# Kernel optimization log

Hardware: AMD Instinct MI355X
Metric: run time of the kernel (lower is better)

## Reference

```python
import jax, jax.numpy as jnp
import numpy as np

N_HIDDEN = 15


def lstm_cell(x, h, c, W_ih, W_hh, b_ih, b_hh):
    # x: [B, in], h/c: [B, H]. PyTorch LSTMCell gate order: i, f, g, o
    gates = x @ W_ih.T + h @ W_hh.T + b_ih + b_hh  # [B, 4H]
    i, f, g, o = jnp.split(gates, 4, axis=-1)
    i = jax.nn.sigmoid(i)
    f = jax.nn.sigmoid(f)
    g = jnp.tanh(g)
    o = jax.nn.sigmoid(o)
    c_new = f * c + i * g
    h_new = o * jnp.tanh(c_new)
    return h_new, c_new


def setup_inputs() -> dict:
    key = jax.random.key(0)
    ks = jax.random.split(key, 12)
    B, T, H = 4096, 1024, N_HIDDEN
    s = 1.0 / np.sqrt(H)  # torch default init bound
    u = lambda k, shape: jax.random.uniform(k, shape, jnp.float32, -s, s)
    return {
        "input": jax.random.normal(ks[0], (B, T), jnp.float32),
        "W_ih1": u(ks[1], (4 * H, 1)),
        "W_hh1": u(ks[2], (4 * H, H)),
        "b_ih1": u(ks[3], (4 * H,)),
        "b_hh1": u(ks[4], (4 * H,)),
        "W_ih2": u(ks[5], (4 * H, H)),
        "W_hh2": u(ks[6], (4 * H, H)),
        "b_ih2": u(ks[7], (4 * H,)),
        "b_hh2": u(ks[8], (4 * H,)),
        "W_lin": u(ks[9], (1, H)),
        "b_lin": u(ks[10], (1,)),
        "future": 64,
    }


def reference(input, W_ih1, W_hh1, b_ih1, b_hh1, W_ih2, W_hh2, b_ih2, b_hh2, W_lin, b_lin, future):
    B = input.shape[0]
    H = N_HIDDEN
    zeros = jnp.zeros((B, H), input.dtype)

    def step(carry, x_t):
        h1, c1, h2, c2 = carry
        h1, c1 = lstm_cell(x_t, h1, c1, W_ih1, W_hh1, b_ih1, b_hh1)
        h2, c2 = lstm_cell(h1, h2, c2, W_ih2, W_hh2, b_ih2, b_hh2)
        out = h2 @ W_lin.T + b_lin  # [B, 1]
        return (h1, c1, h2, c2), out

    xs = input.T[:, :, None]  # [T, B, 1]
    carry, outs = jax.lax.scan(step, (zeros, zeros, zeros, zeros), xs)

    last_out = outs[-1]  # [B, 1]

    def fut_step(carry, _):
        h1, c1, h2, c2, out = carry
        (h1, c1, h2, c2), out = step((h1, c1, h2, c2), out)
        return (h1, c1, h2, c2, out), out

    _, fut_outs = jax.lax.scan(fut_step, (*carry, last_out), None, length=future)

    all_outs = jnp.concatenate([outs, fut_outs], axis=0)  # [T+future, B, 1]
    return all_outs[:, :, 0].T  # [B, T+future]
```

## Files before the change

### kernel.cpp

```cpp
#include <hip/hip_runtime.h>

#define HID   15
#define TMAIN 1024
#define FUT   64
#define OUTW  (TMAIN + FUT)

typedef _Float16 v2h   __attribute__((ext_vector_type(2)));
typedef _Float16 v8h   __attribute__((ext_vector_type(8)));
typedef float    f32x4 __attribute__((ext_vector_type(4)));
typedef int      i32x4 __attribute__((ext_vector_type(4)));

__device__ __forceinline__ float rcp_(float x)  { return __builtin_amdgcn_rcpf(x); }
__device__ __forceinline__ float exp2_(float x) { return __builtin_amdgcn_exp2f(x); }

template<int I> struct ic { static constexpr int v = I; };
template<int J, int N, class F>
__device__ __forceinline__ void unroll_for(F&& f) {
    if constexpr (J < N) { f(ic<J>{}); unroll_for<J + 1, N>(f); }
}

template<int PAT>
__device__ __forceinline__ int swzi(int x) { return __builtin_amdgcn_ds_swizzle(x, PAT); }
template<int PAT>
__device__ __forceinline__ float swzf(float x) { return __int_as_float(swzi<PAT>(__float_as_int(x))); }

__device__ __forceinline__ int bpermi(int addr, int x) { return __builtin_amdgcn_ds_bpermute(addr, x); }
__device__ __forceinline__ float bpermf(int addr, float x) { return __int_as_float(bpermi(addr, __float_as_int(x))); }

template<int CTRL>
__device__ __forceinline__ int dppi(int x) {
    return __builtin_amdgcn_update_dpp(0, x, CTRL, 0xF, 0xF, true);
}

__device__ __forceinline__ v2h pkrtz(float lo, float hi) {
    return __builtin_bit_cast(v2h, __builtin_amdgcn_cvt_pkrtz(lo, hi));
}
__device__ __forceinline__ f32x4 mfma16(v8h a, v8h b, f32x4 c) {
    return __builtin_amdgcn_mfma_f32_16x16x32_f16(a, b, c, 0, 0, 0);
}
template<int I>
__device__ __forceinline__ float xel(const f32x4& a, const f32x4& b) {
    if constexpr (I < 4) return a[I]; else return b[I - 4];
}

__global__ __launch_bounds__(256)
__attribute__((amdgpu_waves_per_eu(1, 1)))
void lstm_seq_kernel(const float* __restrict__ input,
                     const float* __restrict__ W_ih1, const float* __restrict__ W_hh1,
                     const float* __restrict__ b_ih1, const float* __restrict__ b_hh1,
                     const float* __restrict__ W_ih2, const float* __restrict__ W_hh2,
                     const float* __restrict__ b_ih2, const float* __restrict__ b_hh2,
                     const float* __restrict__ W_lin, const float* __restrict__ b_lin,
                     float* __restrict__ out)
{
    const int tid  = threadIdx.x;
    const int wq   = tid >> 6;
    const int lane = tid & 63;
    const int u    = lane >> 4;
    const int c    = lane & 15;
    const int s    = c & 3;
    const int cg   = c >> 2;
    const int b0   = (blockIdx.x * 4 + wq) * 4;

    const float L2E = 1.442695040888963f;
    const float sA[4] = {-L2E, -L2E, -2.0f * L2E, -L2E};
    const float blin = b_lin[0];

    v8h   A1[4], A2[4];
    f32x4 C1[4], C2[4];
    #pragma unroll
    for (int m = 0; m < 4; ++m) {
        #pragma unroll
        for (int e = 0; e < 8; ++e) {
            const int k = (e < 4) ? (4 * u + e) : (16 + 4 * u + (e - 4));
            float v1 = 0.0f, v2 = 0.0f;
            if (c < HID) {
                const int wr = m * HID + c;
                if (k < HID)       { v1 = W_hh1[wr * HID + k]; v2 = W_ih2[wr * HID + k]; }
                else if (k == HID) { v1 = W_ih1[wr]; }
                else if (k >= 16 && k < 16 + HID) { v2 = W_hh2[wr * HID + (k - 16)]; }
            }
            float a2v = sA[m] * v2;
            if (c == 15 && m == 3 && k >= 16 && k < 16 + HID)
                a2v = W_lin[k - 16];
            A1[m][e] = (_Float16)(sA[m] * v1);
            A2[m][e] = (_Float16)a2v;
        }
        #pragma unroll
        for (int r = 0; r < 4; ++r) {
            const int U = 4 * u + r;
            float bv1 = 0.0f, bv2 = 0.0f;
            if (U < HID) {
                bv1 = sA[m] * (b_ih1[m * HID + U] + b_hh1[m * HID + U]);
                bv2 = sA[m] * (b_ih2[m * HID + U] + b_hh2[m * HID + U]);
            }
            if (u == 3 && m == 3 && r == 3) bv2 = blin;
            C1[m][r] = bv1; C2[m][r] = bv2;
        }
    }

    const int   Uown = 4 * u + cg;
    const float wl2  = (Uown < HID) ? W_lin[Uown] : 0.0f;

    const bool cgb0  = (cg & 1) != 0;
    const bool cgb1  = (cg & 2) != 0;
    const bool u3b   = (u == 3);
    const int  a32   = (lane ^ 32) << 2;

    int B0 = 0, B1 = 0;
    int B2s = 0, B3s = 0;
    int B2f = 0, B3f = 0;
    float c1v = 0.0f, c2v = 0.0f;
    float oA = 0.0f, oB = 0.0f;

    auto gsel = [&](const f32x4& q0, const f32x4& q1, const f32x4& q2, const f32x4& q3,
                    float& g0, float& g1, float& g2, float& g3) {
        auto pick = [&](const f32x4& q) -> float {
            const float t0 = cgb0 ? q[1] : q[0];
            const float t1 = cgb0 ? q[3] : q[2];
            return cgb1 ? t1 : t0;
        };
        g0 = pick(q0); g1 = pick(q1); g2 = pick(q2); g3 = pick(q3);
    };

    auto acts = [&](float g0, float g1, float g2, float g3, float& cv) -> float {
        const float Ei = exp2_(g0);
        const float Ef = exp2_(g1);
        const float Eg = exp2_(g2);
        const float Eo = exp2_(g3);
        const float Di = 1.0f + Ei;
        const float Df = 1.0f + Ef;
        const float Dg = 1.0f + Eg;
        const float P  = Di * Dg;
        const float t  = __builtin_fmaf(-Eg, Df, Df);
        const float numer = __builtin_fmaf(cv, P, t);
        cv = numer * rcp_(P * Df);
        const float Y  = exp2_(cv * -2.885390081777927f);
        return (1.0f - Y) * rcp_((1.0f + Y) * (1.0f + Eo));
    };

    auto slots = [&](float h, float& s0, float& s1, float& s2, float& s3) {
        const int hb = __float_as_int(h);
        const float r4  = __int_as_float(dppi<0x114>(hb) | dppi<0x10C>(hb));
        const float r8  = __int_as_float(dppi<0x118>(hb) | dppi<0x108>(hb));
        const float r12 = __int_as_float(dppi<0x11C>(hb) | dppi<0x104>(hb));
        const float A0 = cgb0 ? r4  : h;
        const float A1 = cgb0 ? r12 : r8;
        const float A2 = cgb0 ? h   : r12;
        const float A3 = cgb0 ? r8  : r4;
        s0 = cgb1 ? A1 : A0;
        s1 = cgb1 ? A3 : A2;
        s2 = cgb1 ? A0 : A1;
        s3 = cgb1 ? A2 : A3;
    };

    auto pack01 = [&](float h1n, float xv) {
        float s0, s1, s2, s3; slots(h1n, s0, s1, s2, s3);
        B0 = __builtin_bit_cast(int, pkrtz(s0, s1));
        B1 = __builtin_bit_cast(int, pkrtz(s2, u3b ? xv : s3));
    };
    auto pack23 = [&](float h2n) {
        const int hb = __float_as_int(h2n);
        const float hr = __int_as_float(dppi<0x104>(hb));
        const int p = __builtin_bit_cast(int, pkrtz(h2n, hr));
        B2f = swzi<0x0013>(p);
        B3f = swzi<0x0113>(p);
    };

    auto stash = [&](auto SigC, float ov) {
        constexpr int SIG = decltype(SigC)::v;
        const bool own = (cg == (SIG & 3));
        if constexpr (SIG < 4) oA = own ? ov : oA;
        else                   oB = own ? ov : oB;
    };

    const size_t xadr   = (size_t)(b0 + s) * TMAIN;
    const size_t outb_o = (size_t)(b0 + s) * OUTW;

    auto storeChunk = [&](int chIdx, int baseOff) {
        if (u3b) {
            out[outb_o + baseOff + (size_t)chIdx * 8 + cg]     = oA;
            out[outb_o + baseOff + (size_t)chIdx * 8 + 4 + cg] = oB;
        }
    };

    auto outdot = [&](float h) -> float {
        float pv = wl2 * h;
        pv += swzf<0x101F>(pv);
        pv += swzf<0x201F>(pv);
        pv += swzf<0x401F>(pv);
        pv += bpermf(a32, pv);
        return pv + blin;
    };

    auto iterP = [&](auto Sc, float xv2) {
        constexpr int S = decltype(Sc)::v;
        const v8h Bd = __builtin_bit_cast(v8h, (i32x4){B0, B1, B2s, B3s});
        f32x4 d0 = mfma16(A1[0], Bd, C1[0]);
        f32x4 d1 = mfma16(A1[1], Bd, C1[1]);
        f32x4 d2 = mfma16(A1[2], Bd, C1[2]);
        f32x4 d3 = mfma16(A1[3], Bd, C1[3]);
        const v8h Be = __builtin_bit_cast(v8h, (i32x4){B0, B1, B2f, B3f});
        f32x4 e0 = mfma16(A2[0], Be, C2[0]);
        f32x4 e1 = mfma16(A2[1], Be, C2[1]);
        f32x4 e2 = mfma16(A2[2], Be, C2[2]);
        f32x4 e3 = mfma16(A2[3], Be, C2[3]);

        float P0, P1, P2, P3;
        gsel(d0, d1, d2, d3, P0, P1, P2, P3);
        const float h1n = acts(P0, P1, P2, P3, c1v);
        pack01(h1n, xv2);

        stash(ic<(S + 7) & 7>{}, e3[3]);
        float Q0, Q1, Q2, Q3;
        gsel(e0, e1, e2, e3, Q0, Q1, Q2, Q3);
        const float h2n = acts(Q0, Q1, Q2, Q3, c2v);

        B2s = B2f; B3s = B3f;
        pack23(h2n);
    };

    auto stepS = [&](auto Sc) {
        constexpr int S = decltype(Sc)::v;
        const v8h Bd = __builtin_bit_cast(v8h, (i32x4){B0, B1, B2s, B3s});
        f32x4 d0 = mfma16(A1[0], Bd, C1[0]);
        f32x4 d1 = mfma16(A1[1], Bd, C1[1]);
        f32x4 d2 = mfma16(A1[2], Bd, C1[2]);
        f32x4 d3 = mfma16(A1[3], Bd, C1[3]);
        float P0, P1, P2, P3;
        gsel(d0, d1, d2, d3, P0, P1, P2, P3);
        const float h1n = acts(P0, P1, P2, P3, c1v);
        pack01(h1n, 0.0f);

        const v8h Be = __builtin_bit_cast(v8h, (i32x4){B0, B1, B2f, B3f});
        f32x4 e0 = mfma16(A2[0], Be, C2[0]);
        f32x4 e1 = mfma16(A2[1], Be, C2[1]);
        f32x4 e2 = mfma16(A2[2], Be, C2[2]);
        f32x4 e3 = mfma16(A2[3], Be, C2[3]);
        float Q0, Q1, Q2, Q3;
        gsel(e0, e1, e2, e3, Q0, Q1, Q2, Q3);
        const float h2n = acts(Q0, Q1, Q2, Q3, c2v);

        const float ov = outdot(h2n);
        stash(ic<S>{}, ov);
        const int xb = __builtin_bit_cast(int, pkrtz(0.0f, ov)) & 0xFFFF0000;
        B1 = u3b ? ((B1 & 0xFFFF) | xb) : B1;
        B2s = B2f; B3s = B3f;
        pack23(h2n);
    };

    f32x4 xcA = *(const f32x4*)&input[xadr];
    f32x4 xcB = *(const f32x4*)&input[xadr + 4];
    {
        B0 = 0;
        B1 = u3b ? __builtin_bit_cast(int, pkrtz(0.0f, xcA[0])) : 0;
        const v8h Bv = __builtin_bit_cast(v8h, (i32x4){B0, B1, 0, 0});
        f32x4 d0 = mfma16(A1[0], Bv, C1[0]);
        f32x4 d1 = mfma16(A1[1], Bv, C1[1]);
        f32x4 d2 = mfma16(A1[2], Bv, C1[2]);
        f32x4 d3 = mfma16(A1[3], Bv, C1[3]);
        float P0, P1, P2, P3;
        gsel(d0, d1, d2, d3, P0, P1, P2, P3);
        const float h1n = acts(P0, P1, P2, P3, c1v);
        pack01(h1n, xcA[1]);
        B2s = B3s = B2f = B3f = 0;
    }

    #pragma unroll 1
    for (int ch = 0; ch < 127; ++ch) {
        const f32x4 xnA = *(const f32x4*)&input[xadr + (size_t)(ch + 1) * 8];
        const f32x4 xnB = *(const f32x4*)&input[xadr + (size_t)(ch + 1) * 8 + 4];
        iterP(ic<0>{}, xel<2>(xcA, xcB));
        if (ch > 0) storeChunk(ch - 1, 0);
        iterP(ic<1>{}, xel<3>(xcA, xcB));
        iterP(ic<2>{}, xel<4>(xcA, xcB));
        iterP(ic<3>{}, xel<5>(xcA, xcB));
        iterP(ic<4>{}, xel<6>(xcA, xcB));
        iterP(ic<5>{}, xel<7>(xcA, xcB));
        iterP(ic<6>{}, xnA[0]);
        iterP(ic<7>{}, xnA[1]);
        xcA = xnA; xcB = xnB;
    }

    {
        iterP(ic<0>{}, xel<2>(xcA, xcB));
        storeChunk(126, 0);
        iterP(ic<1>{}, xel<3>(xcA, xcB));
        iterP(ic<2>{}, xel<4>(xcA, xcB));
        iterP(ic<3>{}, xel<5>(xcA, xcB));
        iterP(ic<4>{}, xel<6>(xcA, xcB));
        iterP(ic<5>{}, xel<7>(xcA, xcB));
        iterP(ic<6>{}, 0.0f);

        const v8h Be = __builtin_bit_cast(v8h, (i32x4){B0, B1, B2f, B3f});
        f32x4 e0 = mfma16(A2[0], Be, C2[0]);
        f32x4 e1 = mfma16(A2[1], Be, C2[1]);
        f32x4 e2 = mfma16(A2[2], Be, C2[2]);
        f32x4 e3 = mfma16(A2[3], Be, C2[3]);
        stash(ic<6>{}, e3[3]);
        float Q0, Q1, Q2, Q3;
        gsel(e0, e1, e2, e3, Q0, Q1, Q2, Q3);
        const float h2n = acts(Q0, Q1, Q2, Q3, c2v);
        const float ov23 = outdot(h2n);
        stash(ic<7>{}, ov23);
        storeChunk(127, 0);
        const int xb = __builtin_bit_cast(int, pkrtz(0.0f, ov23)) & 0xFFFF0000;
        B1 = u3b ? ((B1 & 0xFFFF) | xb) : B1;
        B2s = B2f; B3s = B3f;
        pack23(h2n);
    }

    #pragma unroll 1
    for (int fc = 0; fc < FUT / 8; ++fc) {
        unroll_for<0, 8>([&](auto sc) { stepS(sc); });
        storeChunk(fc, TMAIN);
    }
}

extern "C" void kernel_launch(void* const* d_in, const int* in_sizes, int n_in,
                              void* d_out, int out_size, void* d_ws, size_t ws_size,
                              hipStream_t stream)
{
    const float* input = (const float*)d_in[0];
    const float* W_ih1 = (const float*)d_in[1];
    const float* W_hh1 = (const float*)d_in[2];
    const float* b_ih1 = (const float*)d_in[3];
    const float* b_hh1 = (const float*)d_in[4];
    const float* W_ih2 = (const float*)d_in[5];
    const float* W_hh2 = (const float*)d_in[6];
    const float* b_ih2 = (const float*)d_in[7];
    const float* b_hh2 = (const float*)d_in[8];
    const float* W_lin = (const float*)d_in[9];
    const float* b_lin = (const float*)d_in[10];

    lstm_seq_kernel<<<256, 256, 0, stream>>>(
        input, W_ih1, W_hh1, b_ih1, b_hh1,
        W_ih2, W_hh2, b_ih2, b_hh2, W_lin, b_lin,
        (float*)d_out);
}
```

Measured before the change: 415.5 us.

## Split LSTM layers across separate waves with LDS handoff and block barriers

Gives layer 1 and layer 2 their own waves. Layer-1 waves pass the packed h1 and x operands to layer-2 waves through a double-buffered LDS array, with a __syncthreads at every timestep. Each wave now covers half as much work per step, and the grid doubles with two waves per EU, so the two layers should run concurrently instead of serially inside one wave. In exchange it adds a block-wide barrier per step plus LDS round trips, and each output is stored directly per step rather than batched.

```diff
diff --git a/kernel.cpp b/kernel.cpp
--- a/kernel.cpp
+++ b/kernel.cpp
@@ -44,7 +44,7 @@
 }
 
 __global__ __launch_bounds__(256)
-__attribute__((amdgpu_waves_per_eu(1, 1)))
+__attribute__((amdgpu_waves_per_eu(2, 2)))
 void lstm_seq_kernel(const float* __restrict__ input,
                      const float* __restrict__ W_ih1, const float* __restrict__ W_hh1,
                      const float* __restrict__ b_ih1, const float* __restrict__ b_hh1,
@@ -60,7 +60,12 @@
     const int c    = lane & 15;
     const int s    = c & 3;
     const int cg   = c >> 2;
-    const int b0   = (blockIdx.x * 4 + wq) * 4;
+    const bool isA = (wq < 2);
+    const int  g   = wq & 1;
+    const int  b0  = (blockIdx.x * 2 + g) * 4;
+
+    __shared__ long long hbuf[2][2][64];
+    __shared__ float     ovbuf[2][4];
 
     const float L2E = 1.442695040888963f;
     const float sA[4] = {-L2E, -L2E, -2.0f * L2E, -L2E};
@@ -107,11 +112,8 @@
     const bool u3b   = (u == 3);
     const int  a32   = (lane ^ 32) << 2;
 
-    int B0 = 0, B1 = 0;
-    int B2s = 0, B3s = 0;
-    int B2f = 0, B3f = 0;
-    float c1v = 0.0f, c2v = 0.0f;
-    float oA = 0.0f, oB = 0.0f;
+    int B0 = 0, B1 = 0, B0r = 0, B1r = 0, B2 = 0, B3 = 0;
+    float c1v = 0.0f, c2v = 0.0f, h2last = 0.0f;
 
     auto gsel = [&](const f32x4& q0, const f32x4& q1, const f32x4& q2, const f32x4& q3,
                     float& g0, float& g1, float& g2, float& g3) {
@@ -160,28 +162,9 @@
         B1 = __builtin_bit_cast(int, pkrtz(s2, u3b ? xv : s3));
     };
     auto pack23 = [&](float h2n) {
-        const int hb = __float_as_int(h2n);
-        const float hr = __int_as_float(dppi<0x104>(hb));
-        const int p = __builtin_bit_cast(int, pkrtz(h2n, hr));
-        B2f = swzi<0x0013>(p);
-        B3f = swzi<0x0113>(p);
-    };
-
-    auto stash = [&](auto SigC, float ov) {
-        constexpr int SIG = decltype(SigC)::v;
-        const bool own = (cg == (SIG & 3));
-        if constexpr (SIG < 4) oA = own ? ov : oA;
-        else                   oB = own ? ov : oB;
-    };
-
-    const size_t xadr   = (size_t)(b0 + s) * TMAIN;
-    const size_t outb_o = (size_t)(b0 + s) * OUTW;
-
-    auto storeChunk = [&](int chIdx, int baseOff) {
-        if (u3b) {
-            out[outb_o + baseOff + (size_t)chIdx * 8 + cg]     = oA;
-            out[outb_o + baseOff + (size_t)chIdx * 8 + 4 + cg] = oB;
-        }
+        float s0, s1, s2, s3; slots(h2n, s0, s1, s2, s3);
+        B2 = __builtin_bit_cast(int, pkrtz(s0, s1));
+        B3 = __builtin_bit_cast(int, pkrtz(s2, s3));
     };
 
     auto outdot = [&](float h) -> float {
@@ -193,36 +176,21 @@
         return pv + blin;
     };
 
-    auto iterP = [&](auto Sc, float xv2) {
-        constexpr int S = decltype(Sc)::v;
-        const v8h Bd = __builtin_bit_cast(v8h, (i32x4){B0, B1, B2s, B3s});
-        f32x4 d0 = mfma16(A1[0], Bd, C1[0]);
-        f32x4 d1 = mfma16(A1[1], Bd, C1[1]);
-        f32x4 d2 = mfma16(A1[2], Bd, C1[2]);
-        f32x4 d3 = mfma16(A1[3], Bd, C1[3]);
-        const v8h Be = __builtin_bit_cast(v8h, (i32x4){B0, B1, B2f, B3f});
-        f32x4 e0 = mfma16(A2[0], Be, C2[0]);
-        f32x4 e1 = mfma16(A2[1], Be, C2[1]);
-        f32x4 e2 = mfma16(A2[2], Be, C2[2]);
-        f32x4 e3 = mfma16(A2[3], Be, C2[3]);
-
-        float P0, P1, P2, P3;
-        gsel(d0, d1, d2, d3, P0, P1, P2, P3);
-        const float h1n = acts(P0, P1, P2, P3, c1v);
-        pack01(h1n, xv2);
-
-        stash(ic<(S + 7) & 7>{}, e3[3]);
-        float Q0, Q1, Q2, Q3;
-        gsel(e0, e1, e2, e3, Q0, Q1, Q2, Q3);
-        const float h2n = acts(Q0, Q1, Q2, Q3, c2v);
-
-        B2s = B2f; B3s = B3f;
-        pack23(h2n);
-    };
-
-    auto stepS = [&](auto Sc) {
-        constexpr int S = decltype(Sc)::v;
-        const v8h Bd = __builtin_bit_cast(v8h, (i32x4){B0, B1, B2s, B3s});
+    auto pk64 = [&](int lo, int hi) -> long long {
+        return ((long long)(unsigned)hi << 32) | (unsigned)lo;
+    };
+
+    auto runL1 = [&]() -> f32x4* { return nullptr; };
+
+    const size_t xadr   = (size_t)(b0 + s) * TMAIN;
+    const size_t outb_o = (size_t)(b0 + s) * OUTW;
+
+    f32x4 xcA = {0,0,0,0}, xcB = {0,0,0,0};
+    if (isA) {
+        xcA = *(const f32x4*)&input[xadr];
+        xcB = *(const f32x4*)&input[xadr + 4];
+        B1 = u3b ? __builtin_bit_cast(int, pkrtz(0.0f, xcA[0])) : 0;
+        const v8h Bd = __builtin_bit_cast(v8h, (i32x4){B0, B1, 0, 0});
         f32x4 d0 = mfma16(A1[0], Bd, C1[0]);
         f32x4 d1 = mfma16(A1[1], Bd, C1[1]);
         f32x4 d2 = mfma16(A1[2], Bd, C1[2]);
@@ -230,90 +198,107 @@
         float P0, P1, P2, P3;
         gsel(d0, d1, d2, d3, P0, P1, P2, P3);
         const float h1n = acts(P0, P1, P2, P3, c1v);
-        pack01(h1n, 0.0f);
-
-        const v8h Be = __builtin_bit_cast(v8h, (i32x4){B0, B1, B2f, B3f});
-        f32x4 e0 = mfma16(A2[0], Be, C2[0]);
-        f32x4 e1 = mfma16(A2[1], Be, C2[1]);
-        f32x4 e2 = mfma16(A2[2], Be, C2[2]);
-        f32x4 e3 = mfma16(A2[3], Be, C2[3]);
-        float Q0, Q1, Q2, Q3;
-        gsel(e0, e1, e2, e3, Q0, Q1, Q2, Q3);
-        const float h2n = acts(Q0, Q1, Q2, Q3, c2v);
-
-        const float ov = outdot(h2n);
-        stash(ic<S>{}, ov);
-        const int xb = __builtin_bit_cast(int, pkrtz(0.0f, ov)) & 0xFFFF0000;
-        B1 = u3b ? ((B1 & 0xFFFF) | xb) : B1;
-        B2s = B2f; B3s = B3f;
-        pack23(h2n);
-    };
-
-    f32x4 xcA = *(const f32x4*)&input[xadr];
-    f32x4 xcB = *(const f32x4*)&input[xadr + 4];
-    {
-        B0 = 0;
-        B1 = u3b ? __builtin_bit_cast(int, pkrtz(0.0f, xcA[0])) : 0;
-        const v8h Bv = __builtin_bit_cast(v8h, (i32x4){B0, B1, 0, 0});
-        f32x4 d0 = mfma16(A1[0], Bv, C1[0]);
-        f32x4 d1 = mfma16(A1[1], Bv, C1[1]);
-        f32x4 d2 = mfma16(A1[2], Bv, C1[2]);
-        f32x4 d3 = mfma16(A1[3], Bv, C1[3]);
-        float P0, P1, P2, P3;
-        gsel(d0, d1, d2, d3, P0, P1, P2, P3);
-        const float h1n = acts(P0, P1, P2, P3, c1v);
         pack01(h1n, xcA[1]);
-        B2s = B3s = B2f = B3f = 0;
+        hbuf[g][0][lane] = pk64(B0, B1);
     }
 
     #pragma unroll 1
-    for (int ch = 0; ch < 127; ++ch) {
-        const f32x4 xnA = *(const f32x4*)&input[xadr + (size_t)(ch + 1) * 8];
-        const f32x4 xnB = *(const f32x4*)&input[xadr + (size_t)(ch + 1) * 8 + 4];
-        iterP(ic<0>{}, xel<2>(xcA, xcB));
-        if (ch > 0) storeChunk(ch - 1, 0);
-        iterP(ic<1>{}, xel<3>(xcA, xcB));
-        iterP(ic<2>{}, xel<4>(xcA, xcB));
-        iterP(ic<3>{}, xel<5>(xcA, xcB));
-        iterP(ic<4>{}, xel<6>(xcA, xcB));
-        iterP(ic<5>{}, xel<7>(xcA, xcB));
-        iterP(ic<6>{}, xnA[0]);
-        iterP(ic<7>{}, xnA[1]);
-        xcA = xnA; xcB = xnB;
-    }
-
-    {
-        iterP(ic<0>{}, xel<2>(xcA, xcB));
-        storeChunk(126, 0);
-        iterP(ic<1>{}, xel<3>(xcA, xcB));
-        iterP(ic<2>{}, xel<4>(xcA, xcB));
-        iterP(ic<3>{}, xel<5>(xcA, xcB));
-        iterP(ic<4>{}, xel<6>(xcA, xcB));
-        iterP(ic<5>{}, xel<7>(xcA, xcB));
-        iterP(ic<6>{}, 0.0f);
-
-        const v8h Be = __builtin_bit_cast(v8h, (i32x4){B0, B1, B2f, B3f});
-        f32x4 e0 = mfma16(A2[0], Be, C2[0]);
-        f32x4 e1 = mfma16(A2[1], Be, C2[1]);
-        f32x4 e2 = mfma16(A2[2], Be, C2[2]);
-        f32x4 e3 = mfma16(A2[3], Be, C2[3]);
-        stash(ic<6>{}, e3[3]);
-        float Q0, Q1, Q2, Q3;
-        gsel(e0, e1, e2, e3, Q0, Q1, Q2, Q3);
-        const float h2n = acts(Q0, Q1, Q2, Q3, c2v);
-        const float ov23 = outdot(h2n);
-        stash(ic<7>{}, ov23);
-        storeChunk(127, 0);
-        const int xb = __builtin_bit_cast(int, pkrtz(0.0f, ov23)) & 0xFFFF0000;
-        B1 = u3b ? ((B1 & 0xFFFF) | xb) : B1;
-        B2s = B2f; B3s = B3f;
-        pack23(h2n);
+    for (int ch = 0; ch < 128; ++ch) {
+        f32x4 xnA = {0,0,0,0}, xnB = {0,0,0,0};
+        if (isA) {
+            const int chn = (ch < 127) ? ch + 1 : 127;
+            xnA = *(const f32x4*)&input[xadr + (size_t)chn * 8];
+            xnB = *(const f32x4*)&input[xadr + (size_t)chn * 8 + 4];
+        }
+        unroll_for<0, 8>([&](auto sc) {
+            constexpr int S = decltype(sc)::v;
+            __syncthreads();
+            const int t = ch * 8 + S;
+            if (isA) {
+                if ((ch < 127) || (S < 7)) {
+                    const v8h Bd = __builtin_bit_cast(v8h, (i32x4){B0, B1, 0, 0});
+                    f32x4 d0 = mfma16(A1[0], Bd, C1[0]);
+                    f32x4 d1 = mfma16(A1[1], Bd, C1[1]);
+                    f32x4 d2 = mfma16(A1[2], Bd, C1[2]);
+                    f32x4 d3 = mfma16(A1[3], Bd, C1[3]);
+                    float P0, P1, P2, P3;
+                    gsel(d0, d1, d2, d3, P0, P1, P2, P3);
+                    const float h1n = acts(P0, P1, P2, P3, c1v);
+                    float xv2;
+                    if constexpr (S < 6)       xv2 = xel<S + 2>(xcA, xcB);
+                    else if constexpr (S == 6) xv2 = xnA[0];
+                    else                       xv2 = xnA[1];
+                    pack01(h1n, xv2);
+                    hbuf[g][(t + 1) & 1][lane] = pk64(B0, B1);
+                }
+            } else {
+                const long long v = hbuf[g][t & 1][lane];
+                B0r = (int)(unsigned)(v & 0xFFFFFFFFll);
+                B1r = (int)(unsigned)(v >> 32);
+                const v8h Be = __builtin_bit_cast(v8h, (i32x4){B0r, B1r, B2, B3});
+                f32x4 e0 = mfma16(A2[0], Be, C2[0]);
+                f32x4 e1 = mfma16(A2[1], Be, C2[1]);
+                f32x4 e2 = mfma16(A2[2], Be, C2[2]);
+                f32x4 e3 = mfma16(A2[3], Be, C2[3]);
+                if (t > 0 && u3b && cg == 0)
+                    out[outb_o + (t - 1)] = e3[3];
+                float Q0, Q1, Q2, Q3;
+                gsel(e0, e1, e2, e3, Q0, Q1, Q2, Q3);
+                h2last = acts(Q0, Q1, Q2, Q3, c2v);
+                pack23(h2last);
+            }
+        });
+        if (isA) { xcA = xnA; xcB = xnB; }
+    }
+
+    __syncthreads();
+    if (!isA) {
+        const float ov23 = outdot(h2last);
+        if (lane < 4) {
+            ovbuf[g][lane] = ov23;
+            out[(size_t)(b0 + lane) * OUTW + (TMAIN - 1)] = ov23;
+        }
     }
 
     #pragma unroll 1
-    for (int fc = 0; fc < FUT / 8; ++fc) {
-        unroll_for<0, 8>([&](auto sc) { stepS(sc); });
-        storeChunk(fc, TMAIN);
+    for (int f = 0; f < FUT; ++f) {
+        const int t = TMAIN + f;
+        __syncthreads();
+        if (isA) {
+            const float ovp = ovbuf[g][s];
+            const int xb = __builtin_bit_cast(int, pkrtz(0.0f, ovp)) & 0xFFFF0000;
+            B1 = u3b ? ((B1 & 0xFFFF) | xb) : B1;
+            const v8h Bd = __builtin_bit_cast(v8h, (i32x4){B0, B1, 0, 0});
+            f32x4 d0 = mfma16(A1[0], Bd, C1[0]);
+            f32x4 d1 = mfma16(A1[1], Bd, C1[1]);
+            f32x4 d2 = mfma16(A1[2], Bd, C1[2]);
+            f32x4 d3 = mfma16(A1[3], Bd, C1[3]);
+            float P0, P1, P2, P3;
+            gsel(d0, d1, d2, d3, P0, P1, P2, P3);
+            const float h1n = acts(P0, P1, P2, P3, c1v);
+            pack01(h1n, 0.0f);
+            hbuf[g][t & 1][lane] = pk64(B0, B1);
+        }
+        __syncthreads();
+        if (!isA) {
+            const long long v = hbuf[g][t & 1][lane];
+            B0r = (int)(unsigned)(v & 0xFFFFFFFFll);
+            B1r = (int)(unsigned)(v >> 32);
+            const v8h Be = __builtin_bit_cast(v8h, (i32x4){B0r, B1r, B2, B3});
+            f32x4 e0 = mfma16(A2[0], Be, C2[0]);
+            f32x4 e1 = mfma16(A2[1], Be, C2[1]);
+            f32x4 e2 = mfma16(A2[2], Be, C2[2]);
+            f32x4 e3 = mfma16(A2[3], Be, C2[3]);
+            float Q0, Q1, Q2, Q3;
+            gsel(e0, e1, e2, e3, Q0, Q1, Q2, Q3);
+            const float h2n = acts(Q0, Q1, Q2, Q3, c2v);
+            const float ov = outdot(h2n);
+            pack23(h2n);
+            if (lane < 4) {
+                ovbuf[g][lane] = ov;
+                out[(size_t)(b0 + lane) * OUTW + t] = ov;
+            }
+        }
     }
 }
 
@@ -333,7 +318,7 @@
     const float* W_lin = (const float*)d_in[9];
     const float* b_lin = (const float*)d_in[10];
 
-    lstm_seq_kernel<<<256, 256, 0, stream>>>(
+    lstm_seq_kernel<<<512, 256, 0, stream>>>(
         input, W_ih1, W_hh1, b_ih1, b_hh1,
         W_ih2, W_hh2, b_ih2, b_hh2, W_lin, b_lin,
         (float*)d_out);
```

After: 441.7 us. 1.06x slower.
